# Kernel tuning notes

Hardware: AMD Instinct MI355X
Metric: run time of the kernel (lower is better)

Reference implementation:

```python
import jax, jax.numpy as jnp
import numpy as np

N_NODES = 32768
N_GRAPHS = 8
NODES_PER_GRAPH = N_NODES // N_GRAPHS
DEG = 8
N_EDGES = N_NODES * DEG
TW = 25
H = 128
N_LAYERS = 6
L_PDE = 16.0
TMAX = 4.0
DT = 0.04
EPS = 1e-5


def swish(x):
    return x * jax.nn.sigmoid(x)


def _lin(k, fin, fout):
    kw, kb = jax.random.split(k)
    s = 1.0 / np.sqrt(fin)
    return (jax.random.uniform(kw, (fin, fout), minval=-s, maxval=s),
            jax.random.uniform(kb, (fout,), minval=-s, maxval=s))


def _lin_stack(k, n, fin, fout):
    Ws, bs = [], []
    for kk in jax.random.split(k, n):
        W, b = _lin(kk, fin, fout)
        Ws.append(W); bs.append(b)
    return jnp.stack(Ws), jnp.stack(bs)


def setup_inputs() -> dict:
    key = jax.random.key(0)
    ks = jax.random.split(key, 16)
    emb_in = 2 * TW + 2        # 52 = u(50) + pos_x(1) + pos_t(1)
    msg_in = 2 * H + 2 * TW + 2  # 308 = x_i,x_j,u_i-u_j,dpos_x,vars_i
    upd_in = 2 * H + 1          # 257 = x, message, vars
    inp = {}
    inp['u'] = jax.random.normal(ks[0], (N_NODES, 2 * TW), dtype=jnp.float32)
    pos_t = jax.random.uniform(ks[1], (N_NODES, 1)) * TMAX
    pos_x = jax.random.uniform(ks[2], (N_NODES, 1)) * L_PDE
    inp['pos'] = jnp.concatenate([pos_t, pos_x], axis=-1)
    src = jax.random.randint(ks[3], (N_EDGES,), 0, N_NODES)
    dst = jnp.repeat(jnp.arange(N_NODES), DEG)  # every node gets DEG in-edges
    inp['edge_index'] = jnp.stack([src, dst]).astype(jnp.int32)
    inp['batch_idx'] = (jnp.arange(N_NODES) // NODES_PER_GRAPH).astype(jnp.int32)
    inp['emb_W1'], inp['emb_b1'] = _lin(ks[4], emb_in, H)
    inp['emb_W2'], inp['emb_b2'] = _lin(ks[5], H, H)
    inp['msg1_W'], inp['msg1_b'] = _lin_stack(ks[6], N_LAYERS, msg_in, H)
    inp['msg2_W'], inp['msg2_b'] = _lin_stack(ks[7], N_LAYERS, H, H)
    inp['upd1_W'], inp['upd1_b'] = _lin_stack(ks[8], N_LAYERS, upd_in, H)
    inp['upd2_W'], inp['upd2_b'] = _lin_stack(ks[9], N_LAYERS, H, H)
    inp['dbl_W'], inp['dbl_b'] = _lin(ks[10], H, 2 * H)
    kc = jax.random.split(ks[11], 4)
    s1 = 1.0 / np.sqrt(2 * 16)
    inp['conv1_W'] = jax.random.uniform(kc[0], (8, 2, 16), minval=-s1, maxval=s1)
    inp['conv1_b'] = jax.random.uniform(kc[1], (8,), minval=-s1, maxval=s1)
    s2 = 1.0 / np.sqrt(8 * 14)
    inp['conv2_W'] = jax.random.uniform(kc[2], (2, 8, 14), minval=-s2, maxval=s2)
    inp['conv2_b'] = jax.random.uniform(kc[3], (2,), minval=-s2, maxval=s2)
    return inp


def reference(u, pos, edge_index, batch_idx, emb_W1, emb_b1, emb_W2, emb_b2,
              msg1_W, msg1_b, msg2_W, msg2_b, upd1_W, upd1_b, upd2_W, upd2_b,
              dbl_W, dbl_b, conv1_W, conv1_b, conv2_W, conv2_b):
    src, dst = edge_index[0], edge_index[1]  # PyG: x_j = x[src], x_i = x[dst]
    pos_x = pos[:, 1:2] / L_PDE
    pos_t = pos[:, 0:1] / TMAX
    variables = pos_t  # eq_variables == {} -> only pos_t
    node_in = jnp.concatenate([u, pos_x, variables], axis=-1)  # [N,52]
    h = swish(swish(node_in @ emb_W1 + emb_b1) @ emb_W2 + emb_b2)
    ones_e = jnp.ones((src.shape[0], 1), u.dtype)
    counts = jnp.maximum(jax.ops.segment_sum(ones_e, dst, N_NODES), 1.0)
    ones_n = jnp.ones((N_NODES, 1), u.dtype)
    gcounts = jax.ops.segment_sum(ones_n, batch_idx, N_GRAPHS)
    u_d = u[dst] - u[src]
    px_d = pos_x[dst] - pos_x[src]
    var_i = variables[dst]

    def layer(hc, p):
        Wm1, bm1, Wm2, bm2, Wu1, bu1, Wu2, bu2 = p
        edge_in = jnp.concatenate([hc[dst], hc[src], u_d, px_d, var_i], -1)  # [E,308]
        m = swish(edge_in @ Wm1 + bm1)
        m = swish(m @ Wm2 + bm2)
        agg = jax.ops.segment_sum(m, dst, N_NODES) / counts  # mean aggregation
        up = swish(jnp.concatenate([hc, agg, variables], -1) @ Wu1 + bu1)
        up = swish(up @ Wu2 + bu2)
        hn = hc + up  # residual (in_features == out_features)
        gm = jax.ops.segment_sum(hn, batch_idx, N_GRAPHS) / gcounts
        hd = hn - gm[batch_idx]
        gv = jax.ops.segment_sum(hd * hd, batch_idx, N_GRAPHS) / gcounts
        return hd * jax.lax.rsqrt(gv + EPS)[batch_idx], None

    h, _ = jax.lax.scan(layer, h, (msg1_W, msg1_b, msg2_W, msg2_b,
                                   upd1_W, upd1_b, upd2_W, upd2_b))
    x2 = swish(h @ dbl_W + dbl_b).reshape(N_NODES, 2, H)  # double_mlp + Unflatten
    dn = ('NCH', 'OIH', 'NCH')
    y = jax.lax.conv_general_dilated(x2, conv1_W, (3,), 'VALID', dimension_numbers=dn)
    y = swish(y + conv1_b[None, :, None])  # [N,8,38]
    diff = jax.lax.conv_general_dilated(y, conv2_W, (1,), 'VALID', dimension_numbers=dn)
    diff = diff + conv2_b[None, :, None]  # [N,2,25]
    dt_cum = DT * jnp.arange(1, TW + 1, dtype=u.dtype)  # cumsum(dt*ones)
    out = u.reshape(N_NODES, 2, TW) + dt_cum[None, None, :] * diff
    return out.reshape(N_NODES, 2 * TW)
```

## Files before the change

### kernel.cpp

```cpp
#include <hip/hip_runtime.h>
#include <hip/hip_bf16.h>

#define N_NODES 32768
#define N_GRAPHS 8
#define NPG 4096
#define DEG 8
#define N_EDGES (N_NODES*DEG)
#define TW 25
#define NL 6
#define L_PDE 16.0f
#define TMAXC 4.0f
#define DTC 0.04f
#define EPSC 1e-5f

typedef __bf16 bf16x8 __attribute__((ext_vector_type(8)));
typedef float f32x4 __attribute__((ext_vector_type(4)));
typedef unsigned short u16;
typedef unsigned int u32;

__device__ __forceinline__ float bf2f(u16 h){
  union { float f; u32 u; } v; v.u = ((u32)h) << 16; return v.f;
}
__device__ __forceinline__ u16 f2bf(float f){
  union { float f; u32 u; } v; v.f = f;
  u32 r = v.u + 0x7FFFu + ((v.u >> 16) & 1u);
  return (u16)(r >> 16);
}
__device__ __forceinline__ float swishf(float x){
  return x * __builtin_amdgcn_rcpf(1.0f + __expf(-x));
}

__global__ void prep_std(const float* __restrict__ src, u16* __restrict__ dst,
                         int Ksrc, int KPAD, int NOUT)
{
  int l = blockIdx.y;
  int per = KPAD * NOUT;
  int i = blockIdx.x * 256 + threadIdx.x;
  if (i >= per) return;
  int KSTEPS = KPAD / 32;
  int e = i & 7;
  int lane = (i >> 3) & 63;
  int ks = (i >> 9) % KSTEPS;
  int nf = i / (KSTEPS * 512);
  int c = nf * 16 + (lane & 15);
  int k = ks * 32 + (lane >> 4) * 8 + e;
  float v = (k < Ksrc) ? src[(size_t)l * Ksrc * NOUT + (size_t)k * NOUT + c] : 0.f;
  dst[(size_t)l * per + i] = f2bf(v);
}

__global__ void prep_AB(const float* __restrict__ W, const float* __restrict__ bsrc,
                        u16* __restrict__ dst, float* __restrict__ bdst)
{
  int l = blockIdx.y;
  const int KSTEPS = 6;
  int i = blockIdx.x * 256 + threadIdx.x;
  int e = i & 7, lane = (i >> 3) & 63, ks = (i >> 9) % KSTEPS, nf = i / (KSTEPS * 512);
  int c = nf * 16 + (lane & 15);
  int k = ks * 32 + (lane >> 4) * 8 + e;
  const float* Wl = W + (size_t)l * 308 * 128;
  float v = 0.f;
  if (c < 128) {
    int rowi = -1;
    if (k < 128) rowi = k;
    else if (k < 178) rowi = 256 + (k - 128);
    else if (k == 178) rowi = 306;
    else if (k == 179) rowi = 307;
    if (rowi >= 0) v = Wl[rowi * 128 + c];
  } else {
    int cc = c - 128; float sgn = 1.f; int rowi = -1;
    if (k < 128) rowi = 128 + k;
    else if (k < 178) { rowi = 256 + (k - 128); sgn = -1.f; }
    else if (k == 178) { rowi = 306; sgn = -1.f; }
    if (rowi >= 0) v = sgn * Wl[rowi * 128 + cc];
  }
  dst[(size_t)l * 192 * 256 + i] = f2bf(v);
  if (i < 256) bdst[l * 256 + i] = (i < 128) ? bsrc[l * 128 + i] : 0.f;
}

__global__ __launch_bounds__(256) void build_static(
    const float* __restrict__ u, const float* __restrict__ pos,
    u16* __restrict__ X0)
{
  int idx = blockIdx.x * 256 + threadIdx.x;
  int n = idx >> 6, j = idx & 63;
  float v;
  if (j < 50) v = u[n * 50 + j];
  else if (j == 50) v = pos[n * 2 + 1] * (1.f / L_PDE);
  else if (j == 51) v = pos[n * 2 + 0] * (1.f / TMAXC);
  else v = 0.f;
  X0[n * 64 + j] = f2bf(v);
}

template<int KPAD, int NOUT, int ACT, int SMODE, int RESID, int HASOUT>
__global__ __launch_bounds__(256) void gemm2(
    const u16* __restrict__ X, int ldx,
    const u16* __restrict__ Xaux,
    float* hB,
    const float* __restrict__ S1p, const float* __restrict__ S2p,
    const float* __restrict__ pos,
    const u16* __restrict__ Wf, const float* __restrict__ bias,
    u16* __restrict__ out, int ldo,
    float* __restrict__ outF,
    float* __restrict__ S1n, float* __restrict__ S2n)
{
  constexpr int KSTEPS = KPAD / 32;
  constexpr int NF2 = NOUT / 32;
  constexpr int CHUNKS = KPAD / 8;
  constexpr int LDO_S = NOUT + 8;
  constexpr int SMEM_US = 64 * (HASOUT ? (KPAD > LDO_S ? KPAD : LDO_S) : KPAD);
  __shared__ u16 sm[SMEM_US];
  int tid = threadIdx.x, lane = tid & 63, wid = tid >> 6;
  int n0 = blockIdx.x * 64;
  int g = n0 >> 12;

  for (int c = tid; c < 64 * CHUNKS; c += 256) {
    int r = c / CHUNKS, kc = c % CHUNKS;
    int n = n0 + r;
    union { uint4 v; u16 s[8]; } o;
    if (SMODE == 0) {
      o.v = *(const uint4*)(X + (size_t)n * ldx + kc * 8);
    } else {
      if (kc < 16) {
        const float* hp = hB + (size_t)n * 128 + kc * 8;
        float4 a0 = *(const float4*)hp, a1 = *(const float4*)(hp + 4);
        float xv[8] = {a0.x,a0.y,a0.z,a0.w,a1.x,a1.y,a1.z,a1.w};
        if (S1p) {
          #pragma unroll
          for (int j = 0; j < 8; ++j) {
            int cc = kc * 8 + j;
            float m = S1p[g * 128 + cc] * (1.f / NPG);
            float var = S2p[g * 128 + cc] * (1.f / NPG) - m * m;
            xv[j] = (xv[j] - m) * rsqrtf(var + EPSC);
          }
        }
        #pragma unroll
        for (int j = 0; j < 8; ++j) o.s[j] = f2bf(xv[j]);
      } else {
        o.v = *(const uint4*)(Xaux + (size_t)n * 64 + (kc - 16) * 8);
      }
    }
    int byte = r * (KPAD * 2) + kc * 16; byte ^= ((r & 7) << 4);
    *(uint4*)((char*)sm + byte) = o.v;
  }
  __syncthreads();

  int rowHalf = wid & 1, colHalf = wid >> 1;
  f32x4 acc[2][NF2];
  f32x4 zero = {0.f, 0.f, 0.f, 0.f};
  #pragma unroll
  for (int m = 0; m < 2; ++m)
    #pragma unroll
    for (int i = 0; i < NF2; ++i) acc[m][i] = zero;
  int rowA = rowHalf * 32 + (lane & 15);
  int kb = lane >> 4;
  #pragma unroll
  for (int ks = 0; ks < KSTEPS; ++ks) {
    int ab0 = rowA * (KPAD * 2) + ks * 64 + kb * 16; ab0 ^= ((rowA & 7) << 4);
    int rA1 = rowA + 16;
    int ab1 = rA1 * (KPAD * 2) + ks * 64 + kb * 16; ab1 ^= ((rA1 & 7) << 4);
    bf16x8 a0 = *(const bf16x8*)((const char*)sm + ab0);
    bf16x8 a1 = *(const bf16x8*)((const char*)sm + ab1);
    #pragma unroll
    for (int nf2 = 0; nf2 < NF2; ++nf2) {
      bf16x8 b = *(const bf16x8*)(Wf + (((colHalf * NF2 + nf2) * KSTEPS + ks) * 64 + lane) * 8);
      acc[0][nf2] = __builtin_amdgcn_mfma_f32_16x16x32_bf16(a0, b, acc[0][nf2], 0, 0, 0);
      acc[1][nf2] = __builtin_amdgcn_mfma_f32_16x16x32_bf16(a1, b, acc[1][nf2], 0, 0, 0);
    }
  }

  if (HASOUT) __syncthreads();
  #pragma unroll
  for (int nf2 = 0; nf2 < NF2; ++nf2) {
    int col = colHalf * (NOUT / 2) + nf2 * 16 + (lane & 15);
    float bv = bias[col];
    #pragma unroll
    for (int m = 0; m < 2; ++m)
      #pragma unroll
      for (int j = 0; j < 4; ++j) {
        int r = rowHalf * 32 + m * 16 + (lane >> 4) * 4 + j;
        float v = acc[m][nf2][j] + bv;
        if (ACT == 1) v = swishf(v);
        if (HASOUT) sm[r * LDO_S + col] = f2bf(v);
        if (outF) outF[(size_t)(n0 + r) * NOUT + col] = v;
      }
  }
  if (HASOUT) {
    __syncthreads();
    for (int c = tid; c < 64 * NOUT / 8; c += 256) {
      int r = c / (NOUT / 8), kc = c % (NOUT / 8);
      uint4 v = *(const uint4*)(sm + r * LDO_S + kc * 8);
      *(uint4*)(out + (size_t)(n0 + r) * ldo + kc * 8) = v;
    }
  }
}

__global__ __launch_bounds__(256) void enc_fused(
    const u16* __restrict__ X0,
    const u16* __restrict__ W1f, const float* __restrict__ b1,
    const u16* __restrict__ W2f, const float* __restrict__ b2,
    float* __restrict__ hB)
{
  __shared__ u16 s1[64 * 64];
  __shared__ u16 s2[64 * 128];
  int tid = threadIdx.x, lane = tid & 63, wid = tid >> 6;
  int n0 = blockIdx.x * 64;

  for (int c = tid; c < 64 * 8; c += 256) {
    int r = c >> 3, kc = c & 7;
    uint4 v = *(const uint4*)(X0 + (size_t)(n0 + r) * 64 + kc * 8);
    int byte = r * 128 + kc * 16; byte ^= ((r & 7) << 4);
    *(uint4*)((char*)s1 + byte) = v;
  }
  __syncthreads();

  int rowHalf = wid & 1, colHalf = wid >> 1;
  int rowA = rowHalf * 32 + (lane & 15), kb = lane >> 4;
  f32x4 acc[2][4];
  f32x4 zero = {0.f, 0.f, 0.f, 0.f};
  #pragma unroll
  for (int m = 0; m < 2; ++m)
    #pragma unroll
    for (int i = 0; i < 4; ++i) acc[m][i] = zero;
  #pragma unroll
  for (int ks = 0; ks < 2; ++ks) {
    int ab0 = rowA * 128 + ks * 64 + kb * 16; ab0 ^= ((rowA & 7) << 4);
    int rA1 = rowA + 16;
    int ab1 = rA1 * 128 + ks * 64 + kb * 16; ab1 ^= ((rA1 & 7) << 4);
    bf16x8 a0 = *(const bf16x8*)((const char*)s1 + ab0);
    bf16x8 a1 = *(const bf16x8*)((const char*)s1 + ab1);
    #pragma unroll
    for (int nf2 = 0; nf2 < 4; ++nf2) {
      bf16x8 b = *(const bf16x8*)(W1f + (((colHalf * 4 + nf2) * 2 + ks) * 64 + lane) * 8);
      acc[0][nf2] = __builtin_amdgcn_mfma_f32_16x16x32_bf16(a0, b, acc[0][nf2], 0, 0, 0);
      acc[1][nf2] = __builtin_amdgcn_mfma_f32_16x16x32_bf16(a1, b, acc[1][nf2], 0, 0, 0);
    }
  }
  #pragma unroll
  for (int nf2 = 0; nf2 < 4; ++nf2) {
    int col = colHalf * 64 + nf2 * 16 + (lane & 15);
    float bv = b1[col];
    #pragma unroll
    for (int m = 0; m < 2; ++m)
      #pragma unroll
      for (int j = 0; j < 4; ++j) {
        int r = rowHalf * 32 + m * 16 + (lane >> 4) * 4 + j;
        int byte = r * 256 + col * 2; byte ^= ((r & 7) << 4);
        *(u16*)((char*)s2 + byte) = f2bf(swishf(acc[m][nf2][j] + bv));
      }
  }
  __syncthreads();
  #pragma unroll
  for (int m = 0; m < 2; ++m)
    #pragma unroll
    for (int i = 0; i < 4; ++i) acc[m][i] = zero;
  #pragma unroll
  for (int ks = 0; ks < 4; ++ks) {
    int ab0 = rowA * 256 + ks * 64 + kb * 16; ab0 ^= ((rowA & 7) << 4);
    int rA1 = rowA + 16;
    int ab1 = rA1 * 256 + ks * 64 + kb * 16; ab1 ^= ((rA1 & 7) << 4);
    bf16x8 a0 = *(const bf16x8*)((const char*)s2 + ab0);
    bf16x8 a1 = *(const bf16x8*)((const char*)s2 + ab1);
    #pragma unroll
    for (int nf2 = 0; nf2 < 4; ++nf2) {
      bf16x8 b = *(const bf16x8*)(W2f + (((colHalf * 4 + nf2) * 4 + ks) * 64 + lane) * 8);
      acc[0][nf2] = __builtin_amdgcn_mfma_f32_16x16x32_bf16(a0, b, acc[0][nf2], 0, 0, 0);
      acc[1][nf2] = __builtin_amdgcn_mfma_f32_16x16x32_bf16(a1, b, acc[1][nf2], 0, 0, 0);
    }
  }
  #pragma unroll
  for (int nf2 = 0; nf2 < 4; ++nf2) {
    int col = colHalf * 64 + nf2 * 16 + (lane & 15);
    float bv = b2[col];
    #pragma unroll
    for (int m = 0; m < 2; ++m)
      #pragma unroll
      for (int j = 0; j < 4; ++j) {
        int r = rowHalf * 32 + m * 16 + (lane >> 4) * 4 + j;
        hB[(size_t)(n0 + r) * 128 + col] = swishf(acc[m][nf2][j] + bv);
      }
  }
}

__global__ __launch_bounds__(256) void upd_fused(
    const u16* __restrict__ Agg,
    float* hB,
    const float* __restrict__ S1p, const float* __restrict__ S2p,
    const float* __restrict__ pos,
    const u16* __restrict__ W1f, const float* __restrict__ b1,
    const u16* __restrict__ W2f, const float* __restrict__ b2,
    float* __restrict__ S1n, float* __restrict__ S2n)
{
  __shared__ u16 s1[64 * 320];
  __shared__ u16 s2[64 * 128];
  int tid = threadIdx.x, lane = tid & 63, wid = tid >> 6;
  int n0 = blockIdx.x * 64;
  int g = n0 >> 12;

  for (int c = tid; c < 64 * 40; c += 256) {
    int r = c / 40, kc = c % 40;
    int n = n0 + r;
    union { uint4 v; u16 s[8]; } o;
    if (kc < 16) {
      const float* hp = hB + (size_t)n * 128 + kc * 8;
      float4 a0 = *(const float4*)hp, a1 = *(const float4*)(hp + 4);
      float xv[8] = {a0.x,a0.y,a0.z,a0.w,a1.x,a1.y,a1.z,a1.w};
      if (S1p) {
        #pragma unroll
        for (int j = 0; j < 8; ++j) {
          int cc = kc * 8 + j;
          float m = S1p[g * 128 + cc] * (1.f / NPG);
          float var = S2p[g * 128 + cc] * (1.f / NPG) - m * m;
          xv[j] = (xv[j] - m) * rsqrtf(var + EPSC);
        }
      }
      #pragma unroll
      for (int j = 0; j < 8; ++j) o.s[j] = f2bf(xv[j]);
    } else if (kc < 32) {
      o.v = *(const uint4*)(Agg + (size_t)n * 128 + (kc - 16) * 8);
    } else {
      #pragma unroll
      for (int j = 0; j < 8; ++j) o.s[j] = 0;
      if (kc == 32) o.s[0] = f2bf(pos[n * 2] * (1.f / TMAXC));
    }
    int byte = r * 640 + kc * 16; byte ^= ((r & 7) << 4);
    *(uint4*)((char*)s1 + byte) = o.v;
  }
  __syncthreads();

  int rowHalf = wid & 1, colHalf = wid >> 1;
  int rowA = rowHalf * 32 + (lane & 15), kb = lane >> 4;
  f32x4 acc[2][4];
  f32x4 zero = {0.f, 0.f, 0.f, 0.f};
  #pragma unroll
  for (int m = 0; m < 2; ++m)
    #pragma unroll
    for (int i = 0; i < 4; ++i) acc[m][i] = zero;
  #pragma unroll
  for (int ks = 0; ks < 10; ++ks) {
    int ab0 = rowA * 640 + ks * 64 + kb * 16; ab0 ^= ((rowA & 7) << 4);
    int rA1 = rowA + 16;
    int ab1 = rA1 * 640 + ks * 64 + kb * 16; ab1 ^= ((rA1 & 7) << 4);
    bf16x8 a0 = *(const bf16x8*)((const char*)s1 + ab0);
    bf16x8 a1 = *(const bf16x8*)((const char*)s1 + ab1);
    #pragma unroll
    for (int nf2 = 0; nf2 < 4; ++nf2) {
      bf16x8 b = *(const bf16x8*)(W1f + (((colHalf * 4 + nf2) * 10 + ks) * 64 + lane) * 8);
      acc[0][nf2] = __builtin_amdgcn_mfma_f32_16x16x32_bf16(a0, b, acc[0][nf2], 0, 0, 0);
      acc[1][nf2] = __builtin_amdgcn_mfma_f32_16x16x32_bf16(a1, b, acc[1][nf2], 0, 0, 0);
    }
  }
  #pragma unroll
  for (int nf2 = 0; nf2 < 4; ++nf2) {
    int col = colHalf * 64 + nf2 * 16 + (lane & 15);
    float bv = b1[col];
    #pragma unroll
    for (int m = 0; m < 2; ++m)
      #pragma unroll
      for (int j = 0; j < 4; ++j) {
        int r = rowHalf * 32 + m * 16 + (lane >> 4) * 4 + j;
        int byte = r * 256 + col * 2; byte ^= ((r & 7) << 4);
        *(u16*)((char*)s2 + byte) = f2bf(swishf(acc[m][nf2][j] + bv));
      }
  }
  __syncthreads();
  #pragma unroll
  for (int m = 0; m < 2; ++m)
    #pragma unroll
    for (int i = 0; i < 4; ++i) acc[m][i] = zero;
  #pragma unroll
  for (int ks = 0; ks < 4; ++ks) {
    int ab0 = rowA * 256 + ks * 64 + kb * 16; ab0 ^= ((rowA & 7) << 4);
    int rA1 = rowA + 16;
    int ab1 = rA1 * 256 + ks * 64 + kb * 16; ab1 ^= ((rA1 & 7) << 4);
    bf16x8 a0 = *(const bf16x8*)((const char*)s2 + ab0);
    bf16x8 a1 = *(const bf16x8*)((const char*)s2 + ab1);
    #pragma unroll
    for (int nf2 = 0; nf2 < 4; ++nf2) {
      bf16x8 b = *(const bf16x8*)(W2f + (((colHalf * 4 + nf2) * 4 + ks) * 64 + lane) * 8);
      acc[0][nf2] = __builtin_amdgcn_mfma_f32_16x16x32_bf16(a0, b, acc[0][nf2], 0, 0, 0);
      acc[1][nf2] = __builtin_amdgcn_mfma_f32_16x16x32_bf16(a1, b, acc[1][nf2], 0, 0, 0);
    }
  }
  float s1l[4], s2l[4];
  #pragma unroll
  for (int i = 0; i < 4; ++i) { s1l[i] = 0.f; s2l[i] = 0.f; }
  #pragma unroll
  for (int nf2 = 0; nf2 < 4; ++nf2) {
    int col = colHalf * 64 + nf2 * 16 + (lane & 15);
    float bv = b2[col];
    float mm = 0.f, rsig = 1.f;
    if (S1p) {
      mm = S1p[g * 128 + col] * (1.f / NPG);
      float var = S2p[g * 128 + col] * (1.f / NPG) - mm * mm;
      rsig = rsqrtf(var + EPSC);
    }
    #pragma unroll
    for (int m = 0; m < 2; ++m)
      #pragma unroll
      for (int j = 0; j < 4; ++j) {
        int r = rowHalf * 32 + m * 16 + (lane >> 4) * 4 + j;
        int n = n0 + r;
        float v = swishf(acc[m][nf2][j] + bv);
        float hc = hB[(size_t)n * 128 + col];
        hc = (hc - mm) * rsig;
        float hn = hc + v;
        hB[(size_t)n * 128 + col] = hn;
        s1l[nf2] += hn; s2l[nf2] += hn * hn;
      }
  }
  #pragma unroll
  for (int nf2 = 0; nf2 < 4; ++nf2) {
    float s1v = s1l[nf2], s2v = s2l[nf2];
    s1v += __shfl_xor(s1v, 16); s1v += __shfl_xor(s1v, 32);
    s2v += __shfl_xor(s2v, 16); s2v += __shfl_xor(s2v, 32);
    if ((lane >> 4) == 0) {
      int col = colHalf * 64 + nf2 * 16 + (lane & 15);
      atomicAdd(&S1n[g * 128 + col], s1v);
      atomicAdd(&S2n[g * 128 + col], s2v);
    }
  }
}

__global__ __launch_bounds__(256) void msg_kernel(
    const u16* __restrict__ AB, const int* __restrict__ srcIdx,
    const u16* __restrict__ Wf, const float* __restrict__ bm2,
    u16* __restrict__ Agg)
{
  __shared__ u16 Ms[64 * 128];
  __shared__ float aggS[8][132];
  int tid = threadIdx.x, lane = tid & 63, wid = tid >> 6;
  int e0 = blockIdx.x * 64;
  for (int c = tid; c < 1024; c += 256) {
    int i = c >> 4, kc = c & 15;
    int e = e0 + i;
    int nd = e >> 3;
    int ns = srcIdx[e];
    union { uint4 v; u16 s[8]; } va, vb, vo;
    va.v = *(const uint4*)(AB + (size_t)nd * 256 + kc * 8);
    vb.v = *(const uint4*)(AB + (size_t)ns * 256 + 128 + kc * 8);
    #pragma unroll
    for (int j = 0; j < 8; ++j) vo.s[j] = f2bf(swishf(bf2f(va.s[j]) + bf2f(vb.s[j])));
    int byte = i * 256 + kc * 16; byte ^= ((i & 7) << 4);
    *(uint4*)((char*)Ms + byte) = vo.v;
  }
  __syncthreads();
  int rowHalf = wid & 1, colHalf = wid >> 1;
  f32x4 acc[2][4];
  f32x4 zero = {0.f, 0.f, 0.f, 0.f};
  #pragma unroll
  for (int m = 0; m < 2; ++m)
    #pragma unroll
    for (int i = 0; i < 4; ++i) acc[m][i] = zero;
  int rowA = rowHalf * 32 + (lane & 15), kb = lane >> 4;
  #pragma unroll
  for (int ks = 0; ks < 4; ++ks) {
    int ab0 = rowA * 256 + ks * 64 + kb * 16; ab0 ^= ((rowA & 7) << 4);
    int rA1 = rowA + 16;
    int ab1 = rA1 * 256 + ks * 64 + kb * 16; ab1 ^= ((rA1 & 7) << 4);
    bf16x8 a0 = *(const bf16x8*)((const char*)Ms + ab0);
    bf16x8 a1 = *(const bf16x8*)((const char*)Ms + ab1);
    #pragma unroll
    for (int nf2 = 0; nf2 < 4; ++nf2) {
      bf16x8 b = *(const bf16x8*)(Wf + (((colHalf * 4 + nf2) * 4 + ks) * 64 + lane) * 8);
      acc[0][nf2] = __builtin_amdgcn_mfma_f32_16x16x32_bf16(a0, b, acc[0][nf2], 0, 0, 0);
      acc[1][nf2] = __builtin_amdgcn_mfma_f32_16x16x32_bf16(a1, b, acc[1][nf2], 0, 0, 0);
    }
  }
  #pragma unroll
  for (int m = 0; m < 2; ++m)
    #pragma unroll
    for (int nf2 = 0; nf2 < 4; ++nf2) {
      int col = colHalf * 64 + nf2 * 16 + (lane & 15);
      float bv = bm2[col];
      float s = 0.f;
      #pragma unroll
      for (int j = 0; j < 4; ++j) s += swishf(acc[m][nf2][j] + bv);
      s += __shfl_xor(s, 16);
      if ((lane & 31) < 16)
        aggS[rowHalf * 4 + m * 2 + (lane >> 5)][col] = s * 0.125f;
    }
  __syncthreads();
  {
    int node = tid >> 5;
    int c0 = (tid & 31) * 4;
    int n = (e0 >> 3) + node;
    ushort4 o;
    o.x = f2bf(aggS[node][c0 + 0]);
    o.y = f2bf(aggS[node][c0 + 1]);
    o.z = f2bf(aggS[node][c0 + 2]);
    o.w = f2bf(aggS[node][c0 + 3]);
    *(ushort4*)(Agg + (size_t)n * 128 + c0) = o;
  }
}

__global__ __launch_bounds__(256) void dec_conv(
    const float* __restrict__ x2f, const float* __restrict__ u,
    const float* __restrict__ w1, const float* __restrict__ b1,
    const float* __restrict__ w2, const float* __restrict__ b2,
    float* __restrict__ outp)
{
  __shared__ float xs3[2][3][16][44];
  __shared__ float ys[16][8][41];
  __shared__ float w1s[256], w2s[224];
  int tid = threadIdx.x;
  int n0 = blockIdx.x * 16;

  w1s[tid] = w1[tid];
  if (tid < 224) w2s[tid] = w2[tid];
  for (int i = tid; i < 16 * 64; i += 256) {
    int r = i >> 6, cq = i & 63;
    int cc = cq >> 5;
    int j4 = (cq & 31) * 4;
    float4 v = *(const float4*)(x2f + (size_t)(n0 + r) * 256 + cc * 128 + j4);
    float xe[4] = {v.x, v.y, v.z, v.w};
    #pragma unroll
    for (int e = 0; e < 4; ++e) {
      int j = j4 + e;
      xs3[cc][j % 3][r][j / 3] = xe[e];
    }
  }
  __syncthreads();

  {
    int n = tid >> 4, o = (tid >> 1) & 7, th = tid & 1;
    int t0 = th * 19;
    float y[19];
    float b1v = b1[o];
    #pragma unroll
    for (int t = 0; t < 19; ++t) y[t] = b1v;
    #pragma unroll
    for (int cc = 0; cc < 2; ++cc) {
      #pragma unroll
      for (int p = 0; p < 3; ++p) {
        const int KP = (p == 0) ? 6 : 5;
        float wr[6];
        #pragma unroll
        for (int k = 0; k < KP; ++k) wr[k] = w1s[o * 32 + cc * 16 + 3 * k + p];
        float win[24];
        #pragma unroll
        for (int q = 0; q < 18 + KP; ++q) win[q] = xs3[cc][p][n][t0 + q];
        #pragma unroll
        for (int t = 0; t < 19; ++t)
          #pragma unroll
          for (int k = 0; k < KP; ++k)
            y[t] += win[t + k] * wr[k];
      }
    }
    #pragma unroll
    for (int t = 0; t < 19; ++t) ys[n][o][t0 + t] = swishf(y[t]);
  }
  __syncthreads();

  {
    int n = tid >> 4, c = (tid >> 3) & 1, ts = tid & 7;
    int t0 = (ts == 0) ? 0 : ts * 3 + 1;
    int lim = (ts == 0) ? 4 : 3;
    float b2v = b2[c];
    float acc[4] = {b2v, b2v, b2v, b2v};
    #pragma unroll
    for (int ic = 0; ic < 8; ++ic) {
      float wr[14];
      #pragma unroll
      for (int k = 0; k < 14; ++k) wr[k] = w2s[c * 112 + ic * 14 + k];
      float win[17];
      #pragma unroll
      for (int q = 0; q < 17; ++q) win[q] = ys[n][ic][t0 + q];
      #pragma unroll
      for (int t = 0; t < 4; ++t)
        #pragma unroll
        for (int k = 0; k < 14; ++k)
          acc[t] += win[t + k] * wr[k];
    }
    #pragma unroll
    for (int t = 0; t < 4; ++t) {
      if (t < lim) {
        int tt = t0 + t;
        int gi = (n0 + n) * 50 + c * 25 + tt;
        outp[gi] = u[gi] + (DTC * (tt + 1)) * acc[t];
      }
    }
  }
}

extern "C" void kernel_launch(void* const* d_in, const int* in_sizes, int n_in,
                              void* d_out, int out_size, void* d_ws, size_t ws_size,
                              hipStream_t stream) {
  const float* u     = (const float*)d_in[0];
  const float* pos   = (const float*)d_in[1];
  const int*   eidx  = (const int*)d_in[2];
  const float* embW1 = (const float*)d_in[4];
  const float* embb1 = (const float*)d_in[5];
  const float* embW2 = (const float*)d_in[6];
  const float* embb2 = (const float*)d_in[7];
  const float* m1W   = (const float*)d_in[8];
  const float* m1b   = (const float*)d_in[9];
  const float* m2W   = (const float*)d_in[10];
  const float* m2b   = (const float*)d_in[11];
  const float* u1W   = (const float*)d_in[12];
  const float* u1b   = (const float*)d_in[13];
  const float* u2W   = (const float*)d_in[14];
  const float* u2b   = (const float*)d_in[15];
  const float* dblW  = (const float*)d_in[16];
  const float* dblb  = (const float*)d_in[17];
  const float* c1W   = (const float*)d_in[18];
  const float* c1b   = (const float*)d_in[19];
  const float* c2W   = (const float*)d_in[20];
  const float* c2b   = (const float*)d_in[21];
  float* outp = (float*)d_out;
  const int* srcI = eidx;

  char* ws = (char*)d_ws;
  size_t off = 0;
  auto alloc = [&](size_t bytes) -> char* {
    char* p = ws + off; off += (bytes + 255) & ~(size_t)255; return p;
  };
  u16* X0    = (u16*)alloc((size_t)N_NODES * 64 * 2);
  u16* ABbuf = (u16*)alloc((size_t)N_NODES * 256 * 2);
  u16* Agg   = (u16*)alloc((size_t)N_NODES * 128 * 2);
  float* hB  = (float*)alloc((size_t)N_NODES * 128 * 4);
  float* x2f = (float*)alloc((size_t)N_NODES * 256 * 4);
  float* stats = (float*)alloc((size_t)NL * 2 * 1024 * 4);
  u16* WembF1 = (u16*)alloc(64 * 128 * 2);
  u16* WembF2 = (u16*)alloc(128 * 128 * 2);
  u16* WABf   = (u16*)alloc((size_t)6 * 192 * 256 * 2);
  float* bABf = (float*)alloc(6 * 256 * 4);
  u16* Wm2f   = (u16*)alloc((size_t)6 * 128 * 128 * 2);
  u16* Wu1f   = (u16*)alloc((size_t)6 * 320 * 128 * 2);
  u16* Wu2f   = (u16*)alloc((size_t)6 * 128 * 128 * 2);
  u16* Wdblf  = (u16*)alloc((size_t)128 * 256 * 2);

  hipMemsetAsync(stats, 0, (size_t)NL * 2 * 1024 * 4, stream);

  prep_std<<<dim3(32, 1), 256, 0, stream>>>(embW1, WembF1, 52, 64, 128);
  prep_std<<<dim3(64, 1), 256, 0, stream>>>(embW2, WembF2, 128, 128, 128);
  prep_std<<<dim3(64, 6), 256, 0, stream>>>(m2W, Wm2f, 128, 128, 128);
  prep_std<<<dim3(160, 6), 256, 0, stream>>>(u1W, Wu1f, 257, 320, 128);
  prep_std<<<dim3(64, 6), 256, 0, stream>>>(u2W, Wu2f, 128, 128, 128);
  prep_std<<<dim3(128, 1), 256, 0, stream>>>(dblW, Wdblf, 128, 128, 256);
  prep_AB<<<dim3(192, 6), 256, 0, stream>>>(m1W, m1b, WABf, bABf);
  build_static<<<N_NODES * 64 / 256, 256, 0, stream>>>(u, pos, X0);

  enc_fused<<<512, 256, 0, stream>>>(X0, WembF1, embb1, WembF2, embb2, hB);

  for (int l = 0; l < NL; ++l) {
    const float* S1p = l ? stats + (size_t)(l - 1) * 2048 : nullptr;
    const float* S2p = l ? stats + (size_t)(l - 1) * 2048 + 1024 : nullptr;
    float* S1n = stats + (size_t)l * 2048;
    float* S2n = S1n + 1024;
    gemm2<192, 256, 0, 1, 0, 1><<<512, 256, 0, stream>>>(
        nullptr, 0, X0, hB, S1p, S2p, nullptr,
        WABf + (size_t)l * 192 * 256, bABf + l * 256, ABbuf, 256,
        nullptr, nullptr, nullptr);
    msg_kernel<<<N_EDGES / 64, 256, 0, stream>>>(
        ABbuf, srcI, Wm2f + (size_t)l * 128 * 128, m2b + l * 128, Agg);
    upd_fused<<<512, 256, 0, stream>>>(
        Agg, hB, S1p, S2p, pos,
        Wu1f + (size_t)l * 320 * 128, u1b + l * 128,
        Wu2f + (size_t)l * 128 * 128, u2b + l * 128,
        S1n, S2n);
  }

  gemm2<128, 256, 1, 1, 0, 0><<<512, 256, 0, stream>>>(
      nullptr, 0, nullptr, hB, stats + (size_t)5 * 2048, stats + (size_t)5 * 2048 + 1024,
      nullptr, Wdblf, dblb, nullptr, 0, x2f, nullptr, nullptr);
  dec_conv<<<N_NODES / 16, 256, 0, stream>>>(x2f, u, c1W, c1b, c2W, c2b, outp);
}
```

Before: 607.5 us.

## Fuse message kernel into update kernel, keeping aggregates in shared memory

Merges the per-edge message GEMM and mean aggregation into the node-update kernel. Each 64-node block now loops over its 512 in-edges in eight 64-edge steps and writes the aggregated messages straight into the update GEMM's shared-memory input tile, so the global Agg buffer and one kernel launch per layer go away. In exchange the launch grid shrinks from 4096 message blocks to 512 fused blocks. Shared memory per block also grows, which can cut occupancy and leave less parallelism to hide the gather latency.

Measured after the change: 626.6 us. 1.03x slower.

```diff
diff --git a/kernel.cpp b/kernel.cpp
--- a/kernel.cpp
+++ b/kernel.cpp
@@ -281,23 +281,27 @@
   }
 }
 
-__global__ __launch_bounds__(256) void upd_fused(
-    const u16* __restrict__ Agg,
+__global__ __launch_bounds__(256) void msg_upd(
+    const u16* __restrict__ AB, const int* __restrict__ srcIdx,
     float* hB,
     const float* __restrict__ S1p, const float* __restrict__ S2p,
     const float* __restrict__ pos,
+    const u16* __restrict__ Wmf, const float* __restrict__ bm2,
     const u16* __restrict__ W1f, const float* __restrict__ b1,
     const u16* __restrict__ W2f, const float* __restrict__ b2,
     float* __restrict__ S1n, float* __restrict__ S2n)
 {
   __shared__ u16 s1[64 * 320];
+  __shared__ u16 Ms[64 * 128];
   __shared__ u16 s2[64 * 128];
+  __shared__ float aggS[8][132];
   int tid = threadIdx.x, lane = tid & 63, wid = tid >> 6;
   int n0 = blockIdx.x * 64;
   int g = n0 >> 12;
 
   for (int c = tid; c < 64 * 40; c += 256) {
     int r = c / 40, kc = c % 40;
+    if (kc >= 16 && kc < 32) continue;
     int n = n0 + r;
     union { uint4 v; u16 s[8]; } o;
     if (kc < 16) {
@@ -315,8 +319,6 @@
       }
       #pragma unroll
       for (int j = 0; j < 8; ++j) o.s[j] = f2bf(xv[j]);
-    } else if (kc < 32) {
-      o.v = *(const uint4*)(Agg + (size_t)n * 128 + (kc - 16) * 8);
     } else {
       #pragma unroll
       for (int j = 0; j < 8; ++j) o.s[j] = 0;
@@ -325,12 +327,79 @@
     int byte = r * 640 + kc * 16; byte ^= ((r & 7) << 4);
     *(uint4*)((char*)s1 + byte) = o.v;
   }
-  __syncthreads();
 
   int rowHalf = wid & 1, colHalf = wid >> 1;
   int rowA = rowHalf * 32 + (lane & 15), kb = lane >> 4;
+  f32x4 zero = {0.f, 0.f, 0.f, 0.f};
+
+  for (int st = 0; st < 8; ++st) {
+    __syncthreads();
+    int e0 = n0 * 8 + st * 64;
+    for (int c = tid; c < 1024; c += 256) {
+      int i = c >> 4, kc = c & 15;
+      int e = e0 + i;
+      int nd = e >> 3;
+      int ns = srcIdx[e];
+      union { uint4 v; u16 s[8]; } va, vb, vo;
+      va.v = *(const uint4*)(AB + (size_t)nd * 256 + kc * 8);
+      vb.v = *(const uint4*)(AB + (size_t)ns * 256 + 128 + kc * 8);
+      #pragma unroll
+      for (int j = 0; j < 8; ++j) vo.s[j] = f2bf(swishf(bf2f(va.s[j]) + bf2f(vb.s[j])));
+      int byte = i * 256 + kc * 16; byte ^= ((i & 7) << 4);
+      *(uint4*)((char*)Ms + byte) = vo.v;
+    }
+    __syncthreads();
+    {
+      f32x4 acc[2][4];
+      #pragma unroll
+      for (int m = 0; m < 2; ++m)
+        #pragma unroll
+        for (int i = 0; i < 4; ++i) acc[m][i] = zero;
+      #pragma unroll
+      for (int ks = 0; ks < 4; ++ks) {
+        int ab0 = rowA * 256 + ks * 64 + kb * 16; ab0 ^= ((rowA & 7) << 4);
+        int rA1 = rowA + 16;
+        int ab1 = rA1 * 256 + ks * 64 + kb * 16; ab1 ^= ((rA1 & 7) << 4);
+        bf16x8 a0 = *(const bf16x8*)((const char*)Ms + ab0);
+        bf16x8 a1 = *(const bf16x8*)((const char*)Ms + ab1);
+        #pragma unroll
+        for (int nf2 = 0; nf2 < 4; ++nf2) {
+          bf16x8 b = *(const bf16x8*)(Wmf + (((colHalf * 4 + nf2) * 4 + ks) * 64 + lane) * 8);
+          acc[0][nf2] = __builtin_amdgcn_mfma_f32_16x16x32_bf16(a0, b, acc[0][nf2], 0, 0, 0);
+          acc[1][nf2] = __builtin_amdgcn_mfma_f32_16x16x32_bf16(a1, b, acc[1][nf2], 0, 0, 0);
+        }
+      }
+      #pragma unroll
+      for (int m = 0; m < 2; ++m)
+        #pragma unroll
+        for (int nf2 = 0; nf2 < 4; ++nf2) {
+          int col = colHalf * 64 + nf2 * 16 + (lane & 15);
+          float bv = bm2[col];
+          float s = 0.f;
+          #pragma unroll
+          for (int j = 0; j < 4; ++j) s += swishf(acc[m][nf2][j] + bv);
+          s += __shfl_xor(s, 16);
+          if ((lane & 31) < 16)
+            aggS[rowHalf * 4 + m * 2 + (lane >> 5)][col] = s * 0.125f;
+        }
+    }
+    __syncthreads();
+    {
+      int node = tid >> 5;
+      int c0 = (tid & 31) * 4;
+      int r = st * 8 + node;
+      ushort4 o;
+      o.x = f2bf(aggS[node][c0 + 0]);
+      o.y = f2bf(aggS[node][c0 + 1]);
+      o.z = f2bf(aggS[node][c0 + 2]);
+      o.w = f2bf(aggS[node][c0 + 3]);
+      int byte = r * 640 + (128 + c0) * 2; byte ^= ((r & 7) << 4);
+      *(ushort4*)((char*)s1 + byte) = o;
+    }
+  }
+  __syncthreads();
+
   f32x4 acc[2][4];
-  f32x4 zero = {0.f, 0.f, 0.f, 0.f};
   #pragma unroll
   for (int m = 0; m < 2; ++m)
     #pragma unroll
@@ -418,78 +487,6 @@
       atomicAdd(&S1n[g * 128 + col], s1v);
       atomicAdd(&S2n[g * 128 + col], s2v);
     }
-  }
-}
-
-__global__ __launch_bounds__(256) void msg_kernel(
-    const u16* __restrict__ AB, const int* __restrict__ srcIdx,
-    const u16* __restrict__ Wf, const float* __restrict__ bm2,
-    u16* __restrict__ Agg)
-{
-  __shared__ u16 Ms[64 * 128];
-  __shared__ float aggS[8][132];
-  int tid = threadIdx.x, lane = tid & 63, wid = tid >> 6;
-  int e0 = blockIdx.x * 64;
-  for (int c = tid; c < 1024; c += 256) {
-    int i = c >> 4, kc = c & 15;
-    int e = e0 + i;
-    int nd = e >> 3;
-    int ns = srcIdx[e];
-    union { uint4 v; u16 s[8]; } va, vb, vo;
-    va.v = *(const uint4*)(AB + (size_t)nd * 256 + kc * 8);
-    vb.v = *(const uint4*)(AB + (size_t)ns * 256 + 128 + kc * 8);
-    #pragma unroll
-    for (int j = 0; j < 8; ++j) vo.s[j] = f2bf(swishf(bf2f(va.s[j]) + bf2f(vb.s[j])));
-    int byte = i * 256 + kc * 16; byte ^= ((i & 7) << 4);
-    *(uint4*)((char*)Ms + byte) = vo.v;
-  }
-  __syncthreads();
-  int rowHalf = wid & 1, colHalf = wid >> 1;
-  f32x4 acc[2][4];
-  f32x4 zero = {0.f, 0.f, 0.f, 0.f};
-  #pragma unroll
-  for (int m = 0; m < 2; ++m)
-    #pragma unroll
-    for (int i = 0; i < 4; ++i) acc[m][i] = zero;
-  int rowA = rowHalf * 32 + (lane & 15), kb = lane >> 4;
-  #pragma unroll
-  for (int ks = 0; ks < 4; ++ks) {
-    int ab0 = rowA * 256 + ks * 64 + kb * 16; ab0 ^= ((rowA & 7) << 4);
-    int rA1 = rowA + 16;
-    int ab1 = rA1 * 256 + ks * 64 + kb * 16; ab1 ^= ((rA1 & 7) << 4);
-    bf16x8 a0 = *(const bf16x8*)((const char*)Ms + ab0);
-    bf16x8 a1 = *(const bf16x8*)((const char*)Ms + ab1);
-    #pragma unroll
-    for (int nf2 = 0; nf2 < 4; ++nf2) {
-      bf16x8 b = *(const bf16x8*)(Wf + (((colHalf * 4 + nf2) * 4 + ks) * 64 + lane) * 8);
-      acc[0][nf2] = __builtin_amdgcn_mfma_f32_16x16x32_bf16(a0, b, acc[0][nf2], 0, 0, 0);
-      acc[1][nf2] = __builtin_amdgcn_mfma_f32_16x16x32_bf16(a1, b, acc[1][nf2], 0, 0, 0);
-    }
-  }
-  #pragma unroll
-  for (int m = 0; m < 2; ++m)
-    #pragma unroll
-    for (int nf2 = 0; nf2 < 4; ++nf2) {
-      int col = colHalf * 64 + nf2 * 16 + (lane & 15);
-      float bv = bm2[col];
-      float s = 0.f;
-      #pragma unroll
-      for (int j = 0; j < 4; ++j) s += swishf(acc[m][nf2][j] + bv);
-      s += __shfl_xor(s, 16);
-      if ((lane & 31) < 16)
-        aggS[rowHalf * 4 + m * 2 + (lane >> 5)][col] = s * 0.125f;
-    }
-  __syncthreads();
-  {
-    int node = tid >> 5;
-    int c0 = (tid & 31) * 4;
-    int n = (e0 >> 3) + node;
-    ushort4 o;
-    o.x = f2bf(aggS[node][c0 + 0]);
-    o.y = f2bf(aggS[node][c0 + 1]);
-    o.z = f2bf(aggS[node][c0 + 2]);
-    o.w = f2bf(aggS[node][c0 + 3]);
-    *(ushort4*)(Agg + (size_t)n * 128 + c0) = o;
   }
 }
 
@@ -616,7 +613,6 @@
   };
   u16* X0    = (u16*)alloc((size_t)N_NODES * 64 * 2);
   u16* ABbuf = (u16*)alloc((size_t)N_NODES * 256 * 2);
-  u16* Agg   = (u16*)alloc((size_t)N_NODES * 128 * 2);
   float* hB  = (float*)alloc((size_t)N_NODES * 128 * 4);
   float* x2f = (float*)alloc((size_t)N_NODES * 256 * 4);
   float* stats = (float*)alloc((size_t)NL * 2 * 1024 * 4);
@@ -651,10 +647,9 @@
         nullptr, 0, X0, hB, S1p, S2p, nullptr,
         WABf + (size_t)l * 192 * 256, bABf + l * 256, ABbuf, 256,
         nullptr, nullptr, nullptr);
-    msg_kernel<<<N_EDGES / 64, 256, 0, stream>>>(
-        ABbuf, srcI, Wm2f + (size_t)l * 128 * 128, m2b + l * 128, Agg);
-    upd_fused<<<512, 256, 0, stream>>>(
-        Agg, hB, S1p, S2p, pos,
+    msg_upd<<<512, 256, 0, stream>>>(
+        ABbuf, srcI, hB, S1p, S2p, pos,
+        Wm2f + (size_t)l * 128 * 128, m2b + l * 128,
         Wu1f + (size_t)l * 320 * 128, u1b + l * 128,
         Wu2f + (size_t)l * 128 * 128, u2b + l * 128,
         S1n, S2n);
```
